# Performance work log

Hardware: AMD Instinct MI355X
Metric: run time of the kernel (lower is better)

The kernel has to match this reference:

```python
import jax, jax.numpy as jnp
import numpy as np

R = 1          # radius
EPS = 0.01
K = 2 * R + 1  # box kernel size


def boxfilter(x):
    """Replication-pad by R, then depthwise KxK mean filter (groups=C)."""
    xp = jnp.pad(x, ((0, 0), (0, 0), (R, R), (R, R)), mode='edge')
    c = x.shape[1]
    k = jnp.full((c, 1, K, K), 1.0 / (K * K), dtype=x.dtype)
    return jax.lax.conv_general_dilated(
        xp, k, window_strides=(1, 1), padding='VALID',
        feature_group_count=c,
        dimension_numbers=('NCHW', 'OIHW', 'NCHW'))


def _interp_axis(arr, n_in, n_out, axis):
    # bilinear with align_corners=True along one axis
    pos = jnp.linspace(0.0, n_in - 1.0, n_out)
    i0 = jnp.floor(pos).astype(jnp.int32)
    i1 = jnp.minimum(i0 + 1, n_in - 1)
    t = (pos - i0).astype(arr.dtype)
    a0 = jnp.take(arr, i0, axis=axis)
    a1 = jnp.take(arr, i1, axis=axis)
    shp = [1] * arr.ndim
    shp[axis] = n_out
    t = t.reshape(shp)
    return a0 * (1 - t) + a1 * t


def upsample_bilinear(x, H, W):
    _, _, h, w = x.shape
    x = _interp_axis(x, h, H, 2)
    x = _interp_axis(x, w, W, 3)
    return x


def setup_inputs() -> dict:
    key = jax.random.key(0)
    k1, k2, k3 = jax.random.split(key, 3)
    x_lr = jax.random.uniform(k1, (4, 3, 512, 512), dtype=jnp.float32)
    y_lr = jax.random.uniform(k2, (4, 3, 512, 512), dtype=jnp.float32)
    x_hr = jax.random.uniform(k3, (4, 3, 2048, 2048), dtype=jnp.float32)
    return {'x_lr': x_lr, 'y_lr': y_lr, 'x_hr': x_hr}


def reference(x_lr, y_lr, x_hr):
    H, W = x_hr.shape[2], x_hr.shape[3]
    mean_x = boxfilter(x_lr)
    mean_y = boxfilter(y_lr)
    cov_xy = boxfilter(x_lr * y_lr) - mean_x * mean_y
    var_x = boxfilter(x_lr * x_lr) - mean_x * mean_x
    A = cov_xy / (var_x + EPS)
    b = mean_y - A * mean_x
    mean_A = upsample_bilinear(boxfilter(A), H, W)
    mean_b = upsample_bilinear(boxfilter(b), H, W)
    res = jnp.clip(mean_A * x_hr + mean_b, 0.0, 255.0)
    return res.astype(jnp.float32)
```

## Files before the change

### kernel.cpp

```cpp
#include <hip/hip_runtime.h>

#define RAD   1
#define EPS_F 0.01f
#define LR_H  512
#define LR_W  512
#define HR_H  2048
#define HR_W  2048
#define NC    12

#define LR_PLANE (LR_H * LR_W)
#define HR_PLANE (HR_H * HR_W)
#define LR_TOTAL (NC * LR_PLANE)
#define HR_TOTAL (NC * HR_PLANE)

#define TILE 32
#define XT   (TILE + 4)
#define XSTR (XT + 1)
#define AT   (TILE + 2)
#define ASTR (AT + 1)

__global__ void __launch_bounds__(256) k_fused_lr(
    const float* __restrict__ x, const float* __restrict__ y,
    float* __restrict__ mA, float* __restrict__ mb) {
    __shared__ float xs[XT * XSTR];
    __shared__ float ys[XT * XSTR];
    __shared__ float As[AT * ASTR];
    __shared__ float Bs[AT * ASTR];

    int bid = blockIdx.x;
    int p   = bid >> 8;
    int rem = bid & 255;
    int ty  = rem >> 4, tx = rem & 15;
    int oy  = ty * TILE, ox = tx * TILE;
    const float* xp = x + (size_t)p * LR_PLANE;
    const float* yp = y + (size_t)p * LR_PLANE;
    int tid = threadIdx.x;

    for (int i = tid; i < XT * XT; i += 256) {
        int r  = i / XT, c = i - r * XT;
        int gr = min(max(oy + r - 2, 0), LR_H - 1);
        int gc = min(max(ox + c - 2, 0), LR_W - 1);
        xs[r * XSTR + c] = xp[gr * LR_W + gc];
        ys[r * XSTR + c] = yp[gr * LR_W + gc];
    }
    __syncthreads();

    for (int i = tid; i < AT * AT; i += 256) {
        int k  = i / AT, c = i - k * AT;
        int q  = min(max(oy + k - 1, 0), LR_H - 1);
        int pc = min(max(ox + c - 1, 0), LR_W - 1);
        int rows[3] = { max(q - 1, 0)         - oy + 2,
                        q                     - oy + 2,
                        min(q + 1, LR_H - 1)  - oy + 2 };
        int cols[3] = { max(pc - 1, 0)        - ox + 2,
                        pc                    - ox + 2,
                        min(pc + 1, LR_W - 1) - ox + 2 };
        float sx = 0.f, sy = 0.f, sxy = 0.f, sxx = 0.f;
#pragma unroll
        for (int a = 0; a < 3; ++a) {
            int ro = rows[a] * XSTR;
#pragma unroll
            for (int b2 = 0; b2 < 3; ++b2) {
                float xv = xs[ro + cols[b2]];
                float yv = ys[ro + cols[b2]];
                sx  += xv;
                sy  += yv;
                sxy += xv * yv;
                sxx += xv * xv;
            }
        }
        const float inv9 = 1.0f / 9.0f;
        float mx  = sx * inv9;
        float my  = sy * inv9;
        float cov = sxy * inv9 - mx * my;
        float var = sxx * inv9 - mx * mx;
        float Av  = cov / (var + EPS_F);
        As[k * ASTR + c] = Av;
        Bs[k * ASTR + c] = my - Av * mx;
    }
    __syncthreads();

    float* mAp = mA + (size_t)p * LR_PLANE;
    float* mbp = mb + (size_t)p * LR_PLANE;
    for (int i = tid; i < TILE * TILE; i += 256) {
        int r = i >> 5, c = i & 31;
        float sA = 0.f, sB = 0.f;
#pragma unroll
        for (int a = 0; a < 3; ++a) {
            int ro = (r + a) * ASTR + c;
#pragma unroll
            for (int b2 = 0; b2 < 3; ++b2) {
                sA += As[ro + b2];
                sB += Bs[ro + b2];
            }
        }
        const float inv9 = 1.0f / 9.0f;
        mAp[(size_t)(oy + r) * LR_W + (ox + c)] = sA * inv9;
        mbp[(size_t)(oy + r) * LR_W + (ox + c)] = sB * inv9;
    }
}

__global__ void __launch_bounds__(256) k_upsample_fuse(
    const float* __restrict__ mA, const float* __restrict__ mb,
    const float* __restrict__ xhr, float* __restrict__ out) {
    __shared__ float hA[513];
    __shared__ float hb[513];

    int bid = blockIdx.x;
    int i     = bid & (HR_H - 1);
    int plane = bid >> 11;

    const float scale = (float)(LR_H - 1) / (float)(HR_H - 1);

    float ph = i * scale;
    int   i0 = (int)ph;
    int   i1 = min(i0 + 1, LR_H - 1);
    float th = ph - (float)i0;
    float omh = 1.0f - th;

    const float* Ap = mA + (size_t)plane * LR_PLANE;
    const float* bp = mb + (size_t)plane * LR_PLANE;
    int tid = threadIdx.x;

    for (int c = tid; c < 513; c += 256) {
        int col = min(c, LR_W - 1);
        float a0 = Ap[i0 * LR_W + col];
        float a1 = Ap[i1 * LR_W + col];
        float b0 = bp[i0 * LR_W + col];
        float b1 = bp[i1 * LR_W + col];
        hA[c] = a0 * omh + a1 * th;
        hb[c] = b0 * omh + b1 * th;
    }
    __syncthreads();

    const float* xrow = xhr + (size_t)plane * HR_PLANE + (size_t)i * HR_W;
    float*       orow = out + (size_t)plane * HR_PLANE + (size_t)i * HR_W;

#pragma unroll
    for (int g = 0; g < 2; ++g) {
        int j = (tid + g * 256) * 4;
        const float4 xv = *(const float4*)(xrow + j);
        float xin[4] = {xv.x, xv.y, xv.z, xv.w};
        float r[4];
#pragma unroll
        for (int k = 0; k < 4; ++k) {
            float pw = (float)(j + k) * scale;
            int   j0 = (int)pw;
            float tw = pw - (float)j0;
            float omw = 1.0f - tw;
            float a  = hA[j0] * omw + hA[j0 + 1] * tw;
            float bb = hb[j0] * omw + hb[j0 + 1] * tw;
            float v  = a * xin[k] + bb;
            r[k] = fminf(fmaxf(v, 0.0f), 255.0f);
        }
        float4 o;
        o.x = r[0]; o.y = r[1]; o.z = r[2]; o.w = r[3];
        *(float4*)(orow + j) = o;
    }
}

extern "C" void kernel_launch(void* const* d_in, const int* in_sizes, int n_in,
                              void* d_out, int out_size, void* d_ws, size_t ws_size,
                              hipStream_t stream) {
    const float* x_lr = (const float*)d_in[0];
    const float* y_lr = (const float*)d_in[1];
    const float* x_hr = (const float*)d_in[2];
    float* out = (float*)d_out;

    float* mA = (float*)d_ws;
    float* mb = mA + LR_TOTAL;

    {
        int threads = 256;
        int blocks = NC * 16 * 16;
        k_fused_lr<<<blocks, threads, 0, stream>>>(x_lr, y_lr, mA, mb);
    }
    {
        int threads = 256;
        int blocks = NC * HR_H;
        k_upsample_fuse<<<blocks, threads, 0, stream>>>(mA, mb, x_hr, out);
    }
}
```

Baseline: 365.4 us.

## Process four HR rows per block and reuse staged LR rows

The upsample kernel now handles four consecutive high-res rows per block. It stages the three needed low-res rows of A and b in shared memory once and builds four vertically interpolated rows from them. Block indices are also remapped to interleave across 8 groups, probably to spread work across XCDs or caches. This cuts redundant global LR reads and per-block setup, at the cost of fewer blocks, more shared memory and an extra sync.

```diff
diff --git a/kernel.cpp b/kernel.cpp
--- a/kernel.cpp
+++ b/kernel.cpp
@@ -100,62 +100,87 @@
     }
 }
 
-__global__ void __launch_bounds__(256) k_upsample_fuse(
+#define MW    513
+
+__global__ void __launch_bounds__(256) k_upsample_fuse4(
     const float* __restrict__ mA, const float* __restrict__ mb,
     const float* __restrict__ xhr, float* __restrict__ out) {
-    __shared__ float hA[513];
-    __shared__ float hb[513];
+    __shared__ float rawA[3 * MW];
+    __shared__ float rawB[3 * MW];
+    __shared__ float hA[4 * MW];
+    __shared__ float hB[4 * MW];
+
+    const float scale = (float)(LR_H - 1) / (float)(HR_H - 1);
 
     int bid = blockIdx.x;
-    int i     = bid & (HR_H - 1);
-    int plane = bid >> 11;
-
-    const float scale = (float)(LR_H - 1) / (float)(HR_H - 1);
-
-    float ph = i * scale;
-    int   i0 = (int)ph;
-    int   i1 = min(i0 + 1, LR_H - 1);
-    float th = ph - (float)i0;
-    float omh = 1.0f - th;
-
-    const float* Ap = mA + (size_t)plane * LR_PLANE;
-    const float* bp = mb + (size_t)plane * LR_PLANE;
+    int lin = (bid & 7) * 768 + (bid >> 3);
+    int p   = lin >> 9;
+    int rb  = lin & 511;
+    int R   = (int)((float)(4 * rb) * scale);
+
     int tid = threadIdx.x;
-
-    for (int c = tid; c < 513; c += 256) {
-        int col = min(c, LR_W - 1);
-        float a0 = Ap[i0 * LR_W + col];
-        float a1 = Ap[i1 * LR_W + col];
-        float b0 = bp[i0 * LR_W + col];
-        float b1 = bp[i1 * LR_W + col];
-        hA[c] = a0 * omh + a1 * th;
-        hb[c] = b0 * omh + b1 * th;
-    }
-    __syncthreads();
-
-    const float* xrow = xhr + (size_t)plane * HR_PLANE + (size_t)i * HR_W;
-    float*       orow = out + (size_t)plane * HR_PLANE + (size_t)i * HR_W;
-
-#pragma unroll
-    for (int g = 0; g < 2; ++g) {
-        int j = (tid + g * 256) * 4;
-        const float4 xv = *(const float4*)(xrow + j);
-        float xin[4] = {xv.x, xv.y, xv.z, xv.w};
-        float r[4];
-#pragma unroll
-        for (int k = 0; k < 4; ++k) {
-            float pw = (float)(j + k) * scale;
-            int   j0 = (int)pw;
-            float tw = pw - (float)j0;
-            float omw = 1.0f - tw;
-            float a  = hA[j0] * omw + hA[j0 + 1] * tw;
-            float bb = hb[j0] * omw + hb[j0 + 1] * tw;
-            float v  = a * xin[k] + bb;
-            r[k] = fminf(fmaxf(v, 0.0f), 255.0f);
-        }
-        float4 o;
-        o.x = r[0]; o.y = r[1]; o.z = r[2]; o.w = r[3];
-        *(float4*)(orow + j) = o;
+    const float* Ap = mA + (size_t)p * LR_PLANE;
+    const float* bp = mb + (size_t)p * LR_PLANE;
+
+#pragma unroll
+    for (int t = 0; t < 3; ++t) {
+        int rr = min(R + t, LR_H - 1);
+        const float* ar = Ap + rr * LR_W;
+        const float* br = bp + rr * LR_W;
+        for (int c = tid; c < MW; c += 256) {
+            int col = min(c, LR_W - 1);
+            rawA[t * MW + c] = ar[col];
+            rawB[t * MW + c] = br[col];
+        }
+    }
+    __syncthreads();
+
+#pragma unroll
+    for (int k = 0; k < 4; ++k) {
+        int i = 4 * rb + k;
+        float ph = (float)i * scale;
+        int   i0 = (int)ph;
+        float th = ph - (float)i0;
+        int   i1 = min(i0 + 1, LR_H - 1);
+        float omh = 1.0f - th;
+        int r0 = (i0 - R) * MW;
+        int r1 = (i1 - R) * MW;
+        for (int c = tid; c < MW; c += 256) {
+            hA[k * MW + c] = rawA[r0 + c] * omh + rawA[r1 + c] * th;
+            hB[k * MW + c] = rawB[r0 + c] * omh + rawB[r1 + c] * th;
+        }
+    }
+    __syncthreads();
+
+    const size_t hrbase = (size_t)p * HR_PLANE;
+#pragma unroll
+    for (int k = 0; k < 4; ++k) {
+        int i = 4 * rb + k;
+        const float* xrow = xhr + hrbase + (size_t)i * HR_W;
+        float*       orow = out + hrbase + (size_t)i * HR_W;
+        const float* hAr = hA + k * MW;
+        const float* hBr = hB + k * MW;
+#pragma unroll
+        for (int g = 0; g < 2; ++g) {
+            int j = (tid + g * 256) * 4;
+            const float4 xv = *(const float4*)(xrow + j);
+            float xin[4] = {xv.x, xv.y, xv.z, xv.w};
+            float r[4];
+#pragma unroll
+            for (int kk = 0; kk < 4; ++kk) {
+                float pw = (float)(j + kk) * scale;
+                int   j0 = (int)pw;
+                float tw = pw - (float)j0;
+                float omw = 1.0f - tw;
+                float a  = hAr[j0] * omw + hAr[j0 + 1] * tw;
+                float bb = hBr[j0] * omw + hBr[j0 + 1] * tw;
+                float v  = a * xin[kk] + bb;
+                r[kk] = fminf(fmaxf(v, 0.0f), 255.0f);
+            }
+            float4 o;
+            o.x = r[0]; o.y = r[1]; o.z = r[2]; o.w = r[3];
+            *(float4*)(orow + j) = o;
+        }
     }
 }
 
@@ -177,7 +202,7 @@
     }
     {
         int threads = 256;
-        int blocks = NC * HR_H;
-        k_upsample_fuse<<<blocks, threads, 0, stream>>>(mA, mb, x_hr, out);
+        int blocks = NC * (HR_H / 4);
+        k_upsample_fuse4<<<blocks, threads, 0, stream>>>(mA, mb, x_hr, out);
     }
 }
```

Measured after the change: 381.7 us. 4.5% more time.
